# Performance work log

Hardware: AMD Instinct MI355X
Metric: run time of the kernel (lower is better)

Reference implementation:

```python
import jax, jax.numpy as jnp
import numpy as np

D = 1024      # n_embd
NH = 16       # attention heads
E = 8         # n_experts
K = 2         # k_best
FF = 4 * D    # expert MLP hidden
EPS = 1e-6    # rms_norm_epsilon
TEMP = 1.0    # target_temperature


def setup_inputs() -> dict:
    key = jax.random.key(0)
    ks = jax.random.split(key, 12)
    B, S = 2, 1024
    s = 0.02
    return {
        "x": jax.random.normal(ks[0], (B, S, D), jnp.float32),
        "attn_norm_w": jnp.ones((D,), jnp.float32),
        "wq": jax.random.normal(ks[1], (D, D), jnp.float32) * s,
        "wk": jax.random.normal(ks[2], (D, D), jnp.float32) * s,
        "wv": jax.random.normal(ks[3], (D, D), jnp.float32) * s,
        "wo": jax.random.normal(ks[4], (D, D), jnp.float32) * s,
        "mlp_norm_w": jnp.ones((D,), jnp.float32),
        "router_w": jax.random.normal(ks[5], (D, E), jnp.float32) * s,
        "w1": jax.random.normal(ks[6], (E, D, FF), jnp.float32) * s,
        "b1": jnp.zeros((E, FF), jnp.float32),
        "w2": jax.random.normal(ks[7], (E, FF, D), jnp.float32) * s,
        "b2": jnp.zeros((E, D), jnp.float32),
    }


def _rmsnorm(x, w):
    var = jnp.mean(jnp.square(x), axis=-1, keepdims=True)
    return x * jax.lax.rsqrt(var + EPS) * w


def _attention(x, wq, wk, wv, wo):
    B, S, _ = x.shape
    dh = D // NH
    q = (x @ wq).reshape(B, S, NH, dh)
    k = (x @ wk).reshape(B, S, NH, dh)
    v = (x @ wv).reshape(B, S, NH, dh)
    scores = jnp.einsum("bqhd,bkhd->bhqk", q, k) / jnp.sqrt(jnp.float32(dh))
    causal = jnp.tril(jnp.ones((S, S), bool))  # [S,S]
    scores = jnp.where(causal[None, None], scores, jnp.finfo(scores.dtype).min)
    attn = jax.nn.softmax(scores, axis=-1)
    out = jnp.einsum("bhqk,bkhd->bqhd", attn, v).reshape(B, S, D)
    return out @ wo


def reference(x, attn_norm_w, wq, wk, wv, wo, mlp_norm_w, router_w, w1, b1, w2, b2):
    B, S, _ = x.shape
    # attention sub-block
    x = x + _attention(_rmsnorm(x, attn_norm_w), wq, wk, wv, wo)
    residual = x
    h = _rmsnorm(x, mlp_norm_w)  # [B,S,D]

    # router: temperature softmax + top-k
    logits = h @ router_w / TEMP                      # [B,S,E]
    probs = jax.nn.softmax(logits, axis=-1)
    top_k_scores, top_k_indices = jax.lax.top_k(probs, K)  # [B,S,K]
    onehot = jax.nn.one_hot(top_k_indices, E, dtype=h.dtype)  # [B,S,K,E]
    gates = jnp.einsum("bsk,bske->bse", top_k_scores, onehot)  # [B,S,E]

    # load-balancing loss (Switch-style) + expert counts
    counts = jnp.sum(onehot, axis=(0, 1, 2))          # [E]
    frac = counts / (B * S * K)
    mean_prob = jnp.mean(probs, axis=(0, 1))          # [E]
    balancing_loss = E * jnp.sum(frac * mean_prob)

    # experts: dense dispatch; tokens with zero gate contribute nothing,
    # so this matches the sort/gather/scatter top-k combine exactly.
    pre = jnp.einsum("bsd,edf->ebsf", h, w1) + b1[:, None, None]  # [E,B,S,FF]
    act = jax.nn.gelu(pre)
    y = jnp.einsum("ebsf,efd->ebsd", act, w2) + b2[:, None, None]  # [E,B,S,D]
    moe = jnp.einsum("ebsd,bse->bsd", y, gates)

    out = residual + moe
    return out, balancing_loss, counts
```

## Files before the change

### kernel.cpp

```cpp
#include <hip/hip_runtime.h>

typedef __bf16 bf16;
typedef __bf16 bf16x4 __attribute__((ext_vector_type(4)));
typedef __bf16 bf16x8 __attribute__((ext_vector_type(8)));
typedef float f32x4 __attribute__((ext_vector_type(4)));

#define D_   1024
#define S_   1024
#define B_   2
#define NTOK 2048
#define FF_  4096
#define NE   8
#define CAP  5120
#define OUTN 2097152

__device__ __forceinline__ float gelu_f(float x) {
    float u = 0.7978845608028654f * (x + 0.044715f * x * x * x);
    float a = fabsf(u);
    float e = __expf(-2.0f * a);
    float t = (1.0f - e) / (1.0f + e);
    t = copysignf(t, u);
    return 0.5f * x * (1.0f + t);
}

__device__ __forceinline__ void gload16(const void* g, void* l) {
    __builtin_amdgcn_global_load_lds((const __attribute__((address_space(1))) unsigned int*)g,
                                     (__attribute__((address_space(3))) unsigned int*)l,
                                     16, 0, 0);
}

#define VMCNT(n) asm volatile("s_waitcnt vmcnt(" n ")" ::: "memory")
#define BARRIER() do { asm volatile("" ::: "memory"); \
                       __builtin_amdgcn_s_barrier();  \
                       asm volatile("" ::: "memory"); } while (0)

__global__ __launch_bounds__(256) void rmsnorm_k(const float* __restrict__ x,
                                                 const float* __restrict__ w,
                                                 float* __restrict__ yf,
                                                 bf16* __restrict__ yhi,
                                                 bf16* __restrict__ ylo) {
    int row = blockIdx.x;
    int t = threadIdx.x;
    const float* xr = x + (size_t)row * D_;
    float4 v = *(const float4*)(xr + t * 4);
    float ss = v.x * v.x + v.y * v.y + v.z * v.z + v.w * v.w;
    for (int off = 32; off; off >>= 1) ss += __shfl_down(ss, off);
    __shared__ float wsum[4];
    if ((t & 63) == 0) wsum[t >> 6] = ss;
    __syncthreads();
    float tot = wsum[0] + wsum[1] + wsum[2] + wsum[3];
    float rr = rsqrtf(tot * (1.0f / D_) + 1e-6f);
    float4 wv = *(const float4*)(w + t * 4);
    float y[4];
    y[0] = v.x * rr * wv.x; y[1] = v.y * rr * wv.y;
    y[2] = v.z * rr * wv.z; y[3] = v.w * rr * wv.w;
    if (yf) *(float4*)(yf + (size_t)row * D_ + t * 4) = *(float4*)y;
    if (yhi) {
#pragma unroll
        for (int i = 0; i < 4; i++) {
            bf16 hi = (bf16)y[i];
            yhi[(size_t)row * D_ + t * 4 + i] = hi;
            if (ylo) ylo[(size_t)row * D_ + t * 4 + i] = (bf16)(y[i] - (float)hi);
        }
    }
}

__global__ __launch_bounds__(256) void trans_split_k(
    const float* __restrict__ w0, const float* __restrict__ w1p,
    const float* __restrict__ w2p, const float* __restrict__ w3,
    bf16* o0h, bf16* o0l, bf16* o1h, bf16* o1l,
    bf16* o2h, bf16* o2l, bf16* o3h, bf16* o3l) {
    int z = blockIdx.z;
    const float* src = (z == 0) ? w0 : (z == 1) ? w1p : (z == 2) ? w2p : w3;
    bf16* dh = (z == 0) ? o0h : (z == 1) ? o1h : (z == 2) ? o2h : o3h;
    bf16* dl = (z == 0) ? o0l : (z == 1) ? o1l : (z == 2) ? o2l : o3l;
    __shared__ float tl[32][33];
    int c0 = blockIdx.x * 32, r0 = blockIdx.y * 32;
    int tx = threadIdx.x & 31, ty = threadIdx.x >> 5;
#pragma unroll
    for (int i = 0; i < 4; i++) {
        int r = ty + i * 8;
        tl[r][tx] = src[(size_t)(r0 + r) * 1024 + c0 + tx];
    }
    __syncthreads();
#pragma unroll
    for (int i = 0; i < 4; i++) {
        int c = ty + i * 8;
        float v = tl[tx][c];
        bf16 hi = (bf16)v;
        dh[(size_t)(c0 + c) * 1024 + r0 + tx] = hi;
        dl[(size_t)(c0 + c) * 1024 + r0 + tx] = (bf16)(v - (float)hi);
    }
}

__global__ __launch_bounds__(256) void transpose_cast4_k(const float* __restrict__ in,
                                                         bf16* __restrict__ out,
                                                         int R, int C) {
    __shared__ float tl[64][65];
    size_t base = (size_t)blockIdx.z * R * C;
    const float* src = in + base;
    bf16* dst = out + base;
    int c0 = blockIdx.x * 64, r0 = blockIdx.y * 64;
    int t = threadIdx.x;
    int lr = t >> 4;
    int lc = (t & 15) * 4;
#pragma unroll
    for (int i = 0; i < 4; i++) {
        int r = lr + i * 16;
        float4 v = *(const float4*)(src + (size_t)(r0 + r) * C + c0 + lc);
        tl[r][lc] = v.x; tl[r][lc + 1] = v.y; tl[r][lc + 2] = v.z; tl[r][lc + 3] = v.w;
    }
    __syncthreads();
    int wc = t >> 4;
    int wr = (t & 15) * 4;
#pragma unroll
    for (int i = 0; i < 4; i++) {
        int c = wc + i * 16;
        bf16x4 o;
        o[0] = (bf16)tl[wr][c];     o[1] = (bf16)tl[wr + 1][c];
        o[2] = (bf16)tl[wr + 2][c]; o[3] = (bf16)tl[wr + 3][c];
        *(bf16x4*)(dst + (size_t)(c0 + c) * R + r0 + wr) = o;
    }
}

#define SPLIT_STAGE(bi, k0)                             \
    gload16(gah0 + (k0), Lah[bi] + wv * 512);           \
    gload16(gah1 + (k0), Lah[bi] + 2048 + wv * 512);    \
    gload16(gal0 + (k0), Lal[bi] + wv * 512);           \
    gload16(gal1 + (k0), Lal[bi] + 2048 + wv * 512);    \
    gload16(gbh0 + (k0), Lbh[bi] + wv * 512);           \
    gload16(gbh1 + (k0), Lbh[bi] + 2048 + wv * 512);    \
    gload16(gbl0 + (k0), Lbl[bi] + wv * 512);           \
    gload16(gbl1 + (k0), Lbl[bi] + 2048 + wv * 512);

#define SPLIT_COMPUTE(bi) {                                                            \
    bf16x8 fah[4], fal[4], fbh[4], fbl[4];                                             \
    _Pragma("unroll") for (int i = 0; i < 4; i++) {                                    \
        fah[i] = *(const bf16x8*)(Lah[bi] + ra_off[i]);                                \
        fal[i] = *(const bf16x8*)(Lal[bi] + ra_off[i]);                                \
        fbh[i] = *(const bf16x8*)(Lbh[bi] + rb_off[i]);                                \
        fbl[i] = *(const bf16x8*)(Lbl[bi] + rb_off[i]);                                \
    }                                                                                  \
    _Pragma("unroll") for (int mt = 0; mt < 4; mt++)                                   \
    _Pragma("unroll") for (int nt = 0; nt < 4; nt++) {                                 \
        acc[mt][nt] = __builtin_amdgcn_mfma_f32_16x16x32_bf16(fah[mt], fbh[nt], acc[mt][nt], 0, 0, 0); \
        acc[mt][nt] = __builtin_amdgcn_mfma_f32_16x16x32_bf16(fah[mt], fbl[nt], acc[mt][nt], 0, 0, 0); \
        acc[mt][nt] = __builtin_amdgcn_mfma_f32_16x16x32_bf16(fal[mt], fbh[nt], acc[mt][nt], 0, 0, 0); \
    } }

#define SPLIT_STEP(bi, VM)          \
    VMCNT(VM);                      \
    BARRIER();                      \
    SPLIT_COMPUTE(bi);              \
    BARRIER();

#define SPLIT_DECLS(KOFF)                                                              \
    __shared__ __align__(16) bf16 Lah[2][4096];                                        \
    __shared__ __align__(16) bf16 Lal[2][4096];                                        \
    __shared__ __align__(16) bf16 Lbh[2][4096];                                        \
    __shared__ __align__(16) bf16 Lbl[2][4096];                                        \
    int t = threadIdx.x;                                                               \
    int wv = t >> 6, ln = t & 63;                                                      \
    int wm = wv >> 1, wn = wv & 1, l15 = ln & 15, qd = ln >> 4;                        \
    int sr0 = t >> 2, sr1 = 64 + sr0, cl = t & 3;                                      \
    int cs0 = (cl ^ ((sr0 >> 1) & 3)) * 8;                                             \
    int cs1 = (cl ^ ((sr1 >> 1) & 3)) * 8;                                             \
    const bf16* gah0 = Ah + (size_t)(m0 + sr0) * 1024 + (KOFF) + cs0;                  \
    const bf16* gah1 = Ah + (size_t)(m0 + sr1) * 1024 + (KOFF) + cs1;                  \
    const bf16* gal0 = Al + (size_t)(m0 + sr0) * 1024 + (KOFF) + cs0;                  \
    const bf16* gal1 = Al + (size_t)(m0 + sr1) * 1024 + (KOFF) + cs1;                  \
    const bf16* gbh0 = Bh + (size_t)(n0 + sr0) * 1024 + (KOFF) + cs0;                  \
    const bf16* gbh1 = Bh + (size_t)(n0 + sr1) * 1024 + (KOFF) + cs1;                  \
    const bf16* gbl0 = Bl + (size_t)(n0 + sr0) * 1024 + (KOFF) + cs0;                  \
    const bf16* gbl1 = Bl + (size_t)(n0 + sr1) * 1024 + (KOFF) + cs1;                  \
    int ra_off[4], rb_off[4];                                                          \
    _Pragma("unroll") for (int i = 0; i < 4; i++) {                                    \
        int r1 = wm * 64 + i * 16 + l15;                                               \
        ra_off[i] = r1 * 32 + (qd ^ ((r1 >> 1) & 3)) * 8;                              \
        int r2 = wn * 64 + i * 16 + l15;                                               \
        rb_off[i] = r2 * 32 + (qd ^ ((r2 >> 1) & 3)) * 8;                              \
    }                                                                                  \
    f32x4 acc[4][4];                                                                   \
    _Pragma("unroll") for (int mt = 0; mt < 4; mt++)                                   \
    _Pragma("unroll") for (int nt = 0; nt < 4; nt++) acc[mt][nt] = (f32x4){0.f,0.f,0.f,0.f};

__global__ __launch_bounds__(256) void gemm_qkv_k(
    const bf16* __restrict__ Ah, const bf16* __restrict__ Al,
    const bf16* __restrict__ Bqh, const bf16* __restrict__ Bql,
    const bf16* __restrict__ Bkh, const bf16* __restrict__ Bkl,
    const bf16* __restrict__ Bvh, const bf16* __restrict__ Bvl,
    bf16* Cqh, bf16* Cql, bf16* Ckh, bf16* Ckl, bf16* Cvh, bf16* Cvl) {
    int gy = blockIdx.y, zw = gy >> 3;
    const bf16* Bh = (zw == 0) ? Bqh : (zw == 1) ? Bkh : Bvh;
    const bf16* Bl = (zw == 0) ? Bql : (zw == 1) ? Bkl : Bvl;
    bf16* Ch = (zw == 0) ? Cqh : (zw == 1) ? Ckh : Cvh;
    bf16* Cl = (zw == 0) ? Cql : (zw == 1) ? Ckl : Cvl;
    int m0 = blockIdx.x * 128, n0 = (gy & 7) * 128;
    SPLIT_DECLS(0)
    SPLIT_STAGE(0, 0);
    for (int k0 = 0; k0 < 960; k0 += 64) {
        SPLIT_STAGE(1, k0 + 32);
        SPLIT_STEP(0, "8");
        SPLIT_STAGE(0, k0 + 64);
        SPLIT_STEP(1, "8");
    }
    SPLIT_STAGE(1, 992);
    SPLIT_STEP(0, "8");
    SPLIT_STEP(1, "0");
#pragma unroll
    for (int mt = 0; mt < 4; mt++)
#pragma unroll
        for (int nt = 0; nt < 4; nt++)
#pragma unroll
            for (int r = 0; r < 4; r++) {
                int gm = m0 + wm * 64 + mt * 16 + qd * 4 + r;
                int gn = n0 + wn * 64 + nt * 16 + l15;
                float vv = acc[mt][nt][r];
                bf16 hi = (bf16)vv;
                Ch[(size_t)gm * D_ + gn] = hi;
                Cl[(size_t)gm * D_ + gn] = (bf16)(vv - (float)hi);
            }
}

__global__ __launch_bounds__(256) void gemm_wo_k(
    const bf16* __restrict__ Ah, const bf16* __restrict__ Al,
    const bf16* __restrict__ Bh, const bf16* __restrict__ Bl,
    float* __restrict__ C) {
    int m0 = blockIdx.x * 128, n0 = blockIdx.y * 128;
    int kb = blockIdx.z * 256;
    SPLIT_DECLS(kb)
    SPLIT_STAGE(0, 0);
    for (int k0 = 0; k0 < 192; k0 += 64) {
        SPLIT_STAGE(1, k0 + 32);
        SPLIT_STEP(0, "8");
        SPLIT_STAGE(0, k0 + 64);
        SPLIT_STEP(1, "8");
    }
    SPLIT_STAGE(1, 224);
    SPLIT_STEP(0, "8");
    SPLIT_STEP(1, "0");
#pragma unroll
    for (int mt = 0; mt < 4; mt++)
#pragma unroll
        for (int nt = 0; nt < 4; nt++)
#pragma unroll
            for (int r = 0; r < 4; r++) {
                int gm = m0 + wm * 64 + mt * 16 + qd * 4 + r;
                int gn = n0 + wn * 64 + nt * 16 + l15;
                atomicAdd(&C[(size_t)gm * D_ + gn], acc[mt][nt][r]);
            }
}

#define AP 72

__global__ __launch_bounds__(256) void attn_mfma_k(
    const bf16* __restrict__ qhp, const bf16* __restrict__ qlp,
    const bf16* __restrict__ khp, const bf16* __restrict__ klp,
    const bf16* __restrict__ vhp, const bf16* __restrict__ vlp,
    bf16* __restrict__ aoh, bf16* __restrict__ aol) {
    int qt = (int)gridDim.x - 1 - (int)blockIdx.x;
    int h = blockIdx.y, b = blockIdx.z;
    __shared__ bf16 Ksh[64 * AP], Ksl[64 * AP], VTh[64 * AP], VTl[64 * AP];
    __shared__ bf16 Ph[4][16 * AP], Pl[4][16 * AP];
    int t = threadIdx.x, wv = t >> 6, ln = t & 63, l15 = ln & 15, qd = ln >> 4;

    bf16x8 aqh[2], aql[2];
    {
        size_t qb = ((size_t)(b * S_ + qt * 64 + wv * 16 + l15)) * D_ + h * 64 + qd * 8;
        aqh[0] = *(const bf16x8*)(qhp + qb);
        aqh[1] = *(const bf16x8*)(qhp + qb + 32);
        aql[0] = *(const bf16x8*)(qlp + qb);
        aql[1] = *(const bf16x8*)(qlp + qb + 32);
    }
    f32x4 oacc[4];
    float mrow[4], lrow[4];
#pragma unroll
    for (int i = 0; i < 4; i++) {
        oacc[i] = (f32x4){0.f, 0.f, 0.f, 0.f};
        mrow[i] = -1e30f; lrow[i] = 0.0f;
    }

    for (int kt = 0; kt <= qt; kt++) {
        __syncthreads();
#pragma unroll
        for (int j = 0; j < 2; j++) {
            int idx = t + j * 256;
            int row = idx >> 3, ch = (idx & 7) * 8;
            size_t g = ((size_t)(b * S_ + kt * 64 + row)) * D_ + h * 64 + ch;
            *(bf16x8*)&Ksh[row * AP + ch] = *(const bf16x8*)(khp + g);
            *(bf16x8*)&Ksl[row * AP + ch] = *(const bf16x8*)(klp + g);
            bf16x8 vvh = *(const bf16x8*)(vhp + g);
            bf16x8 vvl = *(const bf16x8*)(vlp + g);
#pragma unroll
            for (int jj = 0; jj < 8; jj++) {
                VTh[(ch + jj) * AP + row] = vvh[jj];
                VTl[(ch + jj) * AP + row] = vvl[jj];
            }
        }
        __syncthreads();

        f32x4 sacc[4];
#pragma unroll
        for (int nt = 0; nt < 4; nt++) sacc[nt] = (f32x4){0.f, 0.f, 0.f, 0.f};
#pragma unroll
        for (int ks = 0; ks < 2; ks++) {
#pragma unroll
            for (int nt = 0; nt < 4; nt++) {
                bf16x8 bh = *(const bf16x8*)&Ksh[(nt * 16 + l15) * AP + ks * 32 + qd * 8];
                bf16x8 bl = *(const bf16x8*)&Ksl[(nt * 16 + l15) * AP + ks * 32 + qd * 8];
                sacc[nt] = __builtin_amdgcn_mfma_f32_16x16x32_bf16(aqh[ks], bh, sacc[nt], 0, 0, 0);
                sacc[nt] = __builtin_amdgcn_mfma_f32_16x16x32_bf16(aqh[ks], bl, sacc[nt], 0, 0, 0);
                sacc[nt] = __builtin_amdgcn_mfma_f32_16x16x32_bf16(aql[ks], bh, sacc[nt], 0, 0, 0);
            }
        }
        bool diag = (kt == qt);
#pragma unroll
        for (int r = 0; r < 4; r++) {
            float s0[4];
#pragma unroll
            for (int nt = 0; nt < 4; nt++) {
                s0[nt] = sacc[nt][r] * 0.125f;
                if (diag && (nt * 16 + l15) > (wv * 16 + qd * 4 + r)) s0[nt] = -1e30f;
            }
            float vmax = fmaxf(fmaxf(s0[0], s0[1]), fmaxf(s0[2], s0[3]));
            for (int off = 1; off < 16; off <<= 1) vmax = fmaxf(vmax, __shfl_xor(vmax, off));
            float mnew = fmaxf(mrow[r], vmax);
            float alpha = __expf(mrow[r] - mnew);
            float p[4], rs = 0.0f;
#pragma unroll
            for (int nt = 0; nt < 4; nt++) { p[nt] = __expf(s0[nt] - mnew); rs += p[nt]; }
            for (int off = 1; off < 16; off <<= 1) rs += __shfl_xor(rs, off);
            lrow[r] = lrow[r] * alpha + rs;
            mrow[r] = mnew;
#pragma unroll
            for (int nt = 0; nt < 4; nt++) oacc[nt][r] *= alpha;
            int prow = qd * 4 + r;
#pragma unroll
            for (int nt = 0; nt < 4; nt++) {
                bf16 hi = (bf16)p[nt];
                Ph[wv][prow * AP + nt * 16 + l15] = hi;
                Pl[wv][prow * AP + nt * 16 + l15] = (bf16)(p[nt] - (float)hi);
            }
        }
#pragma unroll
        for (int ks2 = 0; ks2 < 2; ks2++) {
            bf16x8 aph = *(const bf16x8*)&Ph[wv][l15 * AP + ks2 * 32 + qd * 8];
            bf16x8 apl = *(const bf16x8*)&Pl[wv][l15 * AP + ks2 * 32 + qd * 8];
#pragma unroll
            for (int nt = 0; nt < 4; nt++) {
                bf16x8 bvh = *(const bf16x8*)&VTh[(nt * 16 + l15) * AP + ks2 * 32 + qd * 8];
                bf16x8 bvl = *(const bf16x8*)&VTl[(nt * 16 + l15) * AP + ks2 * 32 + qd * 8];
                oacc[nt] = __builtin_amdgcn_mfma_f32_16x16x32_bf16(aph, bvh, oacc[nt], 0, 0, 0);
                oacc[nt] = __builtin_amdgcn_mfma_f32_16x16x32_bf16(aph, bvl, oacc[nt], 0, 0, 0);
                oacc[nt] = __builtin_amdgcn_mfma_f32_16x16x32_bf16(apl, bvh, oacc[nt], 0, 0, 0);
            }
        }
    }

#pragma unroll
    for (int r = 0; r < 4; r++) {
        float inv = 1.0f / lrow[r];
        size_t rowa = ((size_t)(b * S_ + qt * 64 + wv * 16 + qd * 4 + r)) * D_ + h * 64;
#pragma unroll
        for (int nt = 0; nt < 4; nt++) {
            float o = oacc[nt][r] * inv;
            bf16 hi = (bf16)o;
            aoh[rowa + nt * 16 + l15] = hi;
            aol[rowa + nt * 16 + l15] = (bf16)(o - (float)hi);
        }
    }
}

__global__ __launch_bounds__(256) void router_k(const float* __restrict__ h,
                                                const float* __restrict__ rw,
                                                int* __restrict__ tidx,
                                                float* __restrict__ tgate,
                                                int* __restrict__ ecnt,
                                                float* __restrict__ psum) {
    int wv = threadIdx.x >> 6, ln = threadIdx.x & 63;
    int tok = blockIdx.x * 4 + wv;
    const float* hr = h + (size_t)tok * D_;
    float acc[NE];
#pragma unroll
    for (int e = 0; e < NE; e++) acc[e] = 0.0f;
    int base = ln * 16;
#pragma unroll
    for (int c = 0; c < 4; c++) {
        float4 hv = *(const float4*)(hr + base + c * 4);
        const float* rp = rw + (size_t)(base + c * 4) * NE;
        float hx[4] = {hv.x, hv.y, hv.z, hv.w};
#pragma unroll
        for (int jj = 0; jj < 4; jj++)
#pragma unroll
            for (int e = 0; e < NE; e++)
                acc[e] = fmaf(hx[jj], rp[jj * NE + e], acc[e]);
    }
#pragma unroll
    for (int e = 0; e < NE; e++)
        for (int off = 32; off; off >>= 1) acc[e] += __shfl_down(acc[e], off);

    __shared__ float pb[4][NE];
    if (ln == 0) {
        float mx = acc[0];
#pragma unroll
        for (int e = 1; e < NE; e++) mx = fmaxf(mx, acc[e]);
        float p[NE], ssum = 0.0f;
#pragma unroll
        for (int e = 0; e < NE; e++) { p[e] = expf(acc[e] - mx); ssum += p[e]; }
        float inv = 1.0f / ssum;
#pragma unroll
        for (int e = 0; e < NE; e++) p[e] *= inv;
        int i0 = 0; float b0 = p[0];
#pragma unroll
        for (int e = 1; e < NE; e++) if (p[e] > b0) { b0 = p[e]; i0 = e; }
        int i1 = -1; float b1v = -1.0f;
#pragma unroll
        for (int e = 0; e < NE; e++) if (e != i0 && p[e] > b1v) { b1v = p[e]; i1 = e; }
        tidx[tok * 2] = i0; tidx[tok * 2 + 1] = i1;
        tgate[tok * 2] = b0; tgate[tok * 2 + 1] = b1v;
        atomicAdd(&ecnt[i0], 1);
        atomicAdd(&ecnt[i1], 1);
#pragma unroll
        for (int e = 0; e < NE; e++) pb[wv][e] = p[e];
    }
    __syncthreads();
    if (threadIdx.x < NE) {
        float s2 = pb[0][threadIdx.x] + pb[1][threadIdx.x] + pb[2][threadIdx.x] + pb[3][threadIdx.x];
        atomicAdd(&psum[threadIdx.x], s2);
    }
}

__global__ void passb_k(const int* __restrict__ ecnt, const float* __restrict__ psum,
                        int* __restrict__ eoffp, int* __restrict__ ecnt2,
                        float* __restrict__ out_tail) {
    if (threadIdx.x == 0) {
        int off = 0; float loss = 0.0f;
        for (int e = 0; e < NE; e++) {
            eoffp[e] = off;
            int c = ecnt[e];
            off += (c + 127) & ~127;
            loss += (c * (1.0f / 4096.0f)) * (psum[e] * (1.0f / 2048.0f));
            out_tail[1 + e] = (float)c;
            ecnt2[e] = 0;
        }
        eoffp[NE] = off;
        out_tail[0] = 8.0f * loss;
    }
}

__global__ __launch_bounds__(256) void scatter_k(const int* __restrict__ tidx,
                                                 const int* __restrict__ eoffp,
                                                 int* __restrict__ ecnt2,
                                                 int* __restrict__ stok,
                                                 int* __restrict__ sidx) {
    int tok = blockIdx.x * 256 + threadIdx.x;
    for (int k = 0; k < 2; k++) {
        int e = tidx[tok * 2 + k];
        int pos = eoffp[e] + atomicAdd(&ecnt2[e], 1);
        stok[pos] = tok;
        sidx[tok * 2 + k] = pos;
    }
}

#define MOE_STAGE(bufA, bufB, k0)                       \
    gload16(ga0 + (k0), (bufA) + wv * 512);             \
    gload16(ga1 + (k0), (bufA) + 2048 + wv * 512);      \
    gload16(gb0 + (k0), (bufB) + wv * 512);             \
    gload16(gb1 + (k0), (bufB) + 2048 + wv * 512);

#define MOE_TILE(bufA, bufB) {                                                         \
    bf16x8 af[4], bfr[4];                                                              \
    _Pragma("unroll") for (int i = 0; i < 4; i++) {                                    \
        af[i]  = *(const bf16x8*)((bufA) + ra_off[i]);                                 \
        bfr[i] = *(const bf16x8*)((bufB) + rb_off[i]);                                 \
    }                                                                                  \
    _Pragma("unroll") for (int mt = 0; mt < 4; mt++)                                   \
    _Pragma("unroll") for (int nt = 0; nt < 4; nt++)                                   \
        acc[mt][nt] = __builtin_amdgcn_mfma_f32_16x16x32_bf16(af[mt], bfr[nt], acc[mt][nt], 0, 0, 0); }

#define MOE_STEP(rdA, rdB, VM)      \
    VMCNT(VM);                      \
    BARRIER();                      \
    MOE_TILE(rdA, rdB);             \
    BARRIER();

__global__ __launch_bounds__(256) void moe_gemm1_k(const bf16* __restrict__ hB,
                                                   const bf16* __restrict__ w1t,
                                                   const float* __restrict__ b1,
                                                   const int* __restrict__ eoffp,
                                                   const int* __restrict__ stok,
                                                   bf16* __restrict__ act) {
    int m0 = blockIdx.x * 128, n0 = blockIdx.y * 128;
    if (m0 >= eoffp[NE]) return;
    int e = 0;
#pragma unroll
    for (int i = 1; i < NE; i++) if (m0 >= eoffp[i]) e = i;

    __shared__ __align__(16) bf16 As[2][4096];
    __shared__ __align__(16) bf16 Bs[2][4096];
    int t = threadIdx.x;
    int wv = t >> 6, ln = t & 63;
    int wm = wv >> 1, wn = wv & 1, l15 = ln & 15, qd = ln >> 4;

    int sr0 = t >> 2, sr1 = 64 + sr0, cl = t & 3;
    int cs0 = (cl ^ ((sr0 >> 1) & 3)) * 8;
    int cs1 = (cl ^ ((sr1 >> 1) & 3)) * 8;
    const bf16* ga0 = hB + (size_t)stok[m0 + sr0] * D_ + cs0;
    const bf16* ga1 = hB + (size_t)stok[m0 + sr1] * D_ + cs1;
    const bf16* Bb = w1t + ((size_t)e * FF_ + n0) * D_;
    const bf16* gb0 = Bb + (size_t)sr0 * D_ + cs0;
    const bf16* gb1 = Bb + (size_t)sr1 * D_ + cs1;

    int ra_off[4], rb_off[4];
#pragma unroll
    for (int i = 0; i < 4; i++) {
        int r1 = wm * 64 + i * 16 + l15;
        ra_off[i] = r1 * 32 + (qd ^ ((r1 >> 1) & 3)) * 8;
        int r2 = wn * 64 + i * 16 + l15;
        rb_off[i] = r2 * 32 + (qd ^ ((r2 >> 1) & 3)) * 8;
    }

    f32x4 acc[4][4];
#pragma unroll
    for (int mt = 0; mt < 4; mt++)
#pragma unroll
        for (int nt = 0; nt < 4; nt++) acc[mt][nt] = (f32x4){0.f, 0.f, 0.f, 0.f};

    MOE_STAGE(As[0], Bs[0], 0);
    for (int k0 = 0; k0 < 960; k0 += 64) {
        MOE_STAGE(As[1], Bs[1], k0 + 32);
        MOE_STEP(As[0], Bs[0], "4");
        MOE_STAGE(As[0], Bs[0], k0 + 64);
        MOE_STEP(As[1], Bs[1], "4");
    }
    MOE_STAGE(As[1], Bs[1], 992);
    MOE_STEP(As[0], Bs[0], "4");
    MOE_STEP(As[1], Bs[1], "0");

    const float* b1e = b1 + (size_t)e * FF_;
#pragma unroll
    for (int mt = 0; mt < 4; mt++)
#pragma unroll
        for (int nt = 0; nt < 4; nt++) {
            int gn = n0 + wn * 64 + nt * 16 + l15;
            float bias = b1e[gn];
#pragma unroll
            for (int r = 0; r < 4; r++) {
                int gm = m0 + wm * 64 + mt * 16 + qd * 4 + r;
                act[(size_t)gm * FF_ + gn] = (bf16)gelu_f(acc[mt][nt][r] + bias);
            }
        }
}

__global__ __launch_bounds__(256) void moe_gemm2_k(const bf16* __restrict__ act,
                                                   const bf16* __restrict__ w2t,
                                                   const float* __restrict__ b2,
                                                   const int* __restrict__ eoffp,
                                                   float* __restrict__ y) {
    int m0 = blockIdx.x * 128, n0 = blockIdx.y * 128;
    if (m0 >= eoffp[NE]) return;
    int e = 0;
#pragma unroll
    for (int i = 1; i < NE; i++) if (m0 >= eoffp[i]) e = i;

    __shared__ __align__(16) bf16 As[4][4096];
    __shared__ __align__(16) bf16 Bs[4][4096];
    int t = threadIdx.x;
    int wv = t >> 6, ln = t & 63;
    int wm = wv >> 1, wn = wv & 1, l15 = ln & 15, qd = ln >> 4;

    int sr0 = t >> 2, sr1 = 64 + sr0, cl = t & 3;
    int cs0 = (cl ^ ((sr0 >> 1) & 3)) * 8;
    int cs1 = (cl ^ ((sr1 >> 1) & 3)) * 8;
    const bf16* ga0 = act + (size_t)(m0 + sr0) * FF_ + cs0;
    const bf16* ga1 = act + (size_t)(m0 + sr1) * FF_ + cs1;
    const bf16* Bb = w2t + ((size_t)e * D_ + n0) * FF_;
    const bf16* gb0 = Bb + (size_t)sr0 * FF_ + cs0;
    const bf16* gb1 = Bb + (size_t)sr1 * FF_ + cs1;

    int ra_off[4], rb_off[4];
#pragma unroll
    for (int i = 0; i < 4; i++) {
        int r1 = wm * 64 + i * 16 + l15;
        ra_off[i] = r1 * 32 + (qd ^ ((r1 >> 1) & 3)) * 8;
        int r2 = wn * 64 + i * 16 + l15;
        rb_off[i] = r2 * 32 + (qd ^ ((r2 >> 1) & 3)) * 8;
    }

    f32x4 acc[4][4];
#pragma unroll
    for (int mt = 0; mt < 4; mt++)
#pragma unroll
        for (int nt = 0; nt < 4; nt++) acc[mt][nt] = (f32x4){0.f, 0.f, 0.f, 0.f};

    MOE_STAGE(As[0], Bs[0], 0);
    MOE_STAGE(As[1], Bs[1], 32);
    for (int k0 = 0; k0 < 3968; k0 += 128) {
        MOE_STAGE(As[2], Bs[2], k0 + 64);  MOE_STEP(As[0], Bs[0], "8");
        MOE_STAGE(As[3], Bs[3], k0 + 96);  MOE_STEP(As[1], Bs[1], "8");
        MOE_STAGE(As[0], Bs[0], k0 + 128); MOE_STEP(As[2], Bs[2], "8");
        MOE_STAGE(As[1], Bs[1], k0 + 160); MOE_STEP(As[3], Bs[3], "8");
    }
    MOE_STAGE(As[2], Bs[2], 4032); MOE_STEP(As[0], Bs[0], "8");
    MOE_STAGE(As[3], Bs[3], 4064); MOE_STEP(As[1], Bs[1], "8");
    MOE_STEP(As[2], Bs[2], "4");
    MOE_STEP(As[3], Bs[3], "0");

    const float* b2e = b2 + (size_t)e * D_;
#pragma unroll
    for (int mt = 0; mt < 4; mt++)
#pragma unroll
        for (int nt = 0; nt < 4; nt++) {
            int gn = n0 + wn * 64 + nt * 16 + l15;
            float bias = b2e[gn];
#pragma unroll
            for (int r = 0; r < 4; r++) {
                int gm = m0 + wm * 64 + mt * 16 + qd * 4 + r;
                y[(size_t)gm * D_ + gn] = acc[mt][nt][r] + bias;
            }
        }
}

__global__ __launch_bounds__(256) void combine_k(const float* __restrict__ y,
                                                 const int* __restrict__ sidx,
                                                 const float* __restrict__ tgate,
                                                 float* __restrict__ out) {
    int tok = blockIdx.x;
    int d = threadIdx.x * 4;
    int s0 = sidx[tok * 2], s1 = sidx[tok * 2 + 1];
    float g0 = tgate[tok * 2], g1 = tgate[tok * 2 + 1];
    float4 a = *(const float4*)(y + (size_t)s0 * D_ + d);
    float4 b = *(const float4*)(y + (size_t)s1 * D_ + d);
    float4 o = *(const float4*)(out + (size_t)tok * D_ + d);
    o.x += g0 * a.x + g1 * b.x;
    o.y += g0 * a.y + g1 * b.y;
    o.z += g0 * a.z + g1 * b.z;
    o.w += g0 * a.w + g1 * b.w;
    *(float4*)(out + (size_t)tok * D_ + d) = o;
}

extern "C" void kernel_launch(void* const* d_in, const int* in_sizes, int n_in,
                              void* d_out, int out_size, void* d_ws, size_t ws_size,
                              hipStream_t stream) {
    const float* x   = (const float*)d_in[0];
    const float* anw = (const float*)d_in[1];
    const float* wq  = (const float*)d_in[2];
    const float* wk  = (const float*)d_in[3];
    const float* wv  = (const float*)d_in[4];
    const float* wo  = (const float*)d_in[5];
    const float* mnw = (const float*)d_in[6];
    const float* rw  = (const float*)d_in[7];
    const float* w1  = (const float*)d_in[8];
    const float* b1  = (const float*)d_in[9];
    const float* w2  = (const float*)d_in[10];
    const float* b2  = (const float*)d_in[11];
    float* out = (float*)d_out;

    char* p = (char*)d_ws;
    auto take = [&](size_t n) { char* r = p; p += (n + 255) & ~(size_t)255; return r; };
    bf16* h1h = (bf16*)take((size_t)OUTN * 2);
    bf16* h1l = (bf16*)take((size_t)OUTN * 2);
    bf16* qh  = (bf16*)take((size_t)OUTN * 2);
    bf16* ql  = (bf16*)take((size_t)OUTN * 2);
    bf16* kh  = (bf16*)take((size_t)OUTN * 2);
    bf16* kl  = (bf16*)take((size_t)OUTN * 2);
    bf16* vh  = (bf16*)take((size_t)OUTN * 2);
    bf16* vl  = (bf16*)take((size_t)OUTN * 2);
    bf16* wqth = (bf16*)take((size_t)D_ * D_ * 2);
    bf16* wqtl = (bf16*)take((size_t)D_ * D_ * 2);
    bf16* wkth = (bf16*)take((size_t)D_ * D_ * 2);
    bf16* wktl = (bf16*)take((size_t)D_ * D_ * 2);
    bf16* wvth = (bf16*)take((size_t)D_ * D_ * 2);
    bf16* wvtl = (bf16*)take((size_t)D_ * D_ * 2);
    bf16* woth = (bf16*)take((size_t)D_ * D_ * 2);
    bf16* wotl = (bf16*)take((size_t)D_ * D_ * 2);
    bf16* w1t = (bf16*)take((size_t)NE * FF_ * D_ * 2);
    bf16* w2t = (bf16*)take((size_t)NE * FF_ * D_ * 2);
    bf16* act = (bf16*)take((size_t)CAP * FF_ * 2);
    int*   tidx  = (int*)take(NTOK * 2 * 4);
    float* tgate = (float*)take(NTOK * 2 * 4);
    int*   sidx  = (int*)take(NTOK * 2 * 4);
    int*   ecnt  = (int*)take(64);
    int*   ecnt2 = (int*)take(64);
    float* psum  = (float*)take(64);
    int*   eoffp = (int*)take(64);
    int*   stok  = (int*)take(CAP * 4);

    bf16*  aoh = h1h;
    bf16*  aol = h1l;
    float* h_f = (float*)qh;
    bf16*  h_b = kh;
    float* y   = (float*)vh;

    hipMemsetAsync(ecnt, 0, NE * 4, stream);
    hipMemsetAsync(psum, 0, NE * 4, stream);
    hipMemsetAsync(stok, 0, CAP * 4, stream);
    hipMemcpyAsync(out, x, (size_t)OUTN * 4, hipMemcpyDeviceToDevice, stream);

    trans_split_k<<<dim3(32, 32, 4), 256, 0, stream>>>(wq, wk, wv, wo,
        wqth, wqtl, wkth, wktl, wvth, wvtl, woth, wotl);
    transpose_cast4_k<<<dim3(FF_ / 64, D_ / 64, NE), 256, 0, stream>>>(w1, w1t, D_, FF_);
    transpose_cast4_k<<<dim3(D_ / 64, FF_ / 64, NE), 256, 0, stream>>>(w2, w2t, FF_, D_);

    rmsnorm_k<<<NTOK, 256, 0, stream>>>(x, anw, nullptr, h1h, h1l);
    gemm_qkv_k<<<dim3(16, 24), 256, 0, stream>>>(h1h, h1l,
        wqth, wqtl, wkth, wktl, wvth, wvtl, qh, ql, kh, kl, vh, vl);
    attn_mfma_k<<<dim3(16, 16, 2), 256, 0, stream>>>(qh, ql, kh, kl, vh, vl, aoh, aol);
    gemm_wo_k<<<dim3(16, 8, 4), 256, 0, stream>>>(aoh, aol, woth, wotl, out);

    rmsnorm_k<<<NTOK, 256, 0, stream>>>(out, mnw, h_f, h_b, nullptr);
    router_k<<<NTOK / 4, 256, 0, stream>>>(h_f, rw, tidx, tgate, ecnt, psum);
    passb_k<<<1, 64, 0, stream>>>(ecnt, psum, eoffp, ecnt2, out + OUTN);
    scatter_k<<<NTOK / 256, 256, 0, stream>>>(tidx, eoffp, ecnt2, stok, sidx);
    moe_gemm1_k<<<dim3(CAP / 128, FF_ / 128), 256, 0, stream>>>(h_b, w1t, b1, eoffp, stok, act);
    moe_gemm2_k<<<dim3(CAP / 128, D_ / 128), 256, 0, stream>>>(act, w2t, b2, eoffp, y);
    combine_k<<<NTOK, 256, 0, stream>>>(y, sidx, tgate, out);
}
```

Measured before the change: 776.1 us.

## Pre-transpose V and use direct global-to-LDS swizzled loads in attention

Adds a separate kernel that writes V hi/lo in a transposed [b,h,d,s] layout. The attention kernel then loads K and transposed V tiles straight into LDS with gload16 and an XOR-swizzled layout, replacing the register-staged scalar transpose stores and the padded layout. This removes per-element LDS scatter writes and bank conflicts in the inner loop, at the cost of an extra kernel launch and about 8 MB of extra global traffic for the transposed V buffers.

```diff
diff --git a/kernel.cpp b/kernel.cpp
--- a/kernel.cpp
+++ b/kernel.cpp
@@ -120,6 +120,36 @@
         o[0] = (bf16)tl[wr][c];     o[1] = (bf16)tl[wr + 1][c];
         o[2] = (bf16)tl[wr + 2][c]; o[3] = (bf16)tl[wr + 3][c];
         *(bf16x4*)(dst + (size_t)(c0 + c) * R + r0 + wr) = o;
+    }
+}
+
+__global__ __launch_bounds__(256) void vtrans_k(const bf16* __restrict__ vh,
+                                                const bf16* __restrict__ vl,
+                                                bf16* __restrict__ vth,
+                                                bf16* __restrict__ vtl) {
+    int s0 = blockIdx.x * 64;
+    int bh = blockIdx.y;
+    int b = bh >> 4, h = bh & 15;
+    const bf16* src = blockIdx.z ? vl : vh;
+    bf16* dst = blockIdx.z ? vtl : vth;
+    __shared__ bf16 tl[64][65];
+    int t = threadIdx.x;
+    int lr = t >> 4, lc = (t & 15) * 4;
+#pragma unroll
+    for (int i = 0; i < 4; i++) {
+        int r = lr + i * 16;
+        bf16x4 v = *(const bf16x4*)(src + (size_t)(b * S_ + s0 + r) * D_ + h * 64 + lc);
+        tl[r][lc] = v[0]; tl[r][lc + 1] = v[1]; tl[r][lc + 2] = v[2]; tl[r][lc + 3] = v[3];
+    }
+    __syncthreads();
+    int wc = t >> 4, wr = (t & 15) * 4;
+#pragma unroll
+    for (int i = 0; i < 4; i++) {
+        int c = wc + i * 16;
+        bf16x4 o;
+        o[0] = tl[wr][c];     o[1] = tl[wr + 1][c];
+        o[2] = tl[wr + 2][c]; o[3] = tl[wr + 3][c];
+        *(bf16x4*)(dst + (size_t)(bh * 64 + c) * S_ + s0 + wr) = o;
     }
 }
 
@@ -256,11 +286,11 @@
 __global__ __launch_bounds__(256) void attn_mfma_k(
     const bf16* __restrict__ qhp, const bf16* __restrict__ qlp,
     const bf16* __restrict__ khp, const bf16* __restrict__ klp,
-    const bf16* __restrict__ vhp, const bf16* __restrict__ vlp,
+    const bf16* __restrict__ vth, const bf16* __restrict__ vtl,
     bf16* __restrict__ aoh, bf16* __restrict__ aol) {
     int qt = (int)gridDim.x - 1 - (int)blockIdx.x;
     int h = blockIdx.y, b = blockIdx.z;
-    __shared__ bf16 Ksh[64 * AP], Ksl[64 * AP], VTh[64 * AP], VTl[64 * AP];
+    __shared__ __align__(16) bf16 Ksh[4096], Ksl[4096], VTh[4096], VTl[4096];
     __shared__ bf16 Ph[4][16 * AP], Pl[4][16 * AP];
     int t = threadIdx.x, wv = t >> 6, ln = t & 63, l15 = ln & 15, qd = ln >> 4;
 
@@ -272,6 +302,27 @@
         aql[0] = *(const bf16x8*)(qlp + qb);
         aql[1] = *(const bf16x8*)(qlp + qb + 32);
     }
+
+    int srow = t >> 3, scl = t & 7;
+    int gsc = (scl ^ (srow & 7)) * 8;
+    const bf16* kh0 = khp + (size_t)(b * S_ + srow) * D_ + h * 64 + gsc;
+    const bf16* kh1 = khp + (size_t)(b * S_ + srow + 32) * D_ + h * 64 + gsc;
+    const bf16* kl0 = klp + (size_t)(b * S_ + srow) * D_ + h * 64 + gsc;
+    const bf16* kl1 = klp + (size_t)(b * S_ + srow + 32) * D_ + h * 64 + gsc;
+    const bf16* vt0 = vth + (size_t)((b * 16 + h) * 64 + srow) * S_ + gsc;
+    const bf16* vt1 = vth + (size_t)((b * 16 + h) * 64 + srow + 32) * S_ + gsc;
+    const bf16* wl0 = vtl + (size_t)((b * 16 + h) * 64 + srow) * S_ + gsc;
+    const bf16* wl1 = vtl + (size_t)((b * 16 + h) * 64 + srow + 32) * S_ + gsc;
+
+    int soff[4][2];
+#pragma unroll
+    for (int nt = 0; nt < 4; nt++)
+#pragma unroll
+        for (int ks = 0; ks < 2; ks++) {
+            int r = nt * 16 + l15;
+            soff[nt][ks] = r * 64 + ((ks * 4 + qd) ^ (r & 7)) * 8;
+        }
+
     f32x4 oacc[4];
     float mrow[4], lrow[4];
 #pragma unroll
@@ -281,23 +332,15 @@
     }
 
     for (int kt = 0; kt <= qt; kt++) {
-        __syncthreads();
-#pragma unroll
-        for (int j = 0; j < 2; j++) {
-            int idx = t + j * 256;
-            int row = idx >> 3, ch = (idx & 7) * 8;
-            size_t g = ((size_t)(b * S_ + kt * 64 + row)) * D_ + h * 64 + ch;
-            *(bf16x8*)&Ksh[row * AP + ch] = *(const bf16x8*)(khp + g);
-            *(bf16x8*)&Ksl[row * AP + ch] = *(const bf16x8*)(klp + g);
-            bf16x8 vvh = *(const bf16x8*)(vhp + g);
-            bf16x8 vvl = *(const bf16x8*)(vlp + g);
-#pragma unroll
-            for (int jj = 0; jj < 8; jj++) {
-                VTh[(ch + jj) * AP + row] = vvh[jj];
-                VTl[(ch + jj) * AP + row] = vvl[jj];
-            }
-        }
-        __syncthreads();
+        BARRIER();
+        size_t ko = (size_t)kt * 64 * D_;
+        int vo = kt * 64;
+        gload16(kh0 + ko, Ksh + wv * 512); gload16(kh1 + ko, Ksh + 2048 + wv * 512);
+        gload16(kl0 + ko, Ksl + wv * 512); gload16(kl1 + ko, Ksl + 2048 + wv * 512);
+        gload16(vt0 + vo, VTh + wv * 512); gload16(vt1 + vo, VTh + 2048 + wv * 512);
+        gload16(wl0 + vo, VTl + wv * 512); gload16(wl1 + vo, VTl + 2048 + wv * 512);
+        VMCNT("0");
+        BARRIER();
 
         f32x4 sacc[4];
 #pragma unroll
@@ -306,8 +349,8 @@
         for (int ks = 0; ks < 2; ks++) {
 #pragma unroll
             for (int nt = 0; nt < 4; nt++) {
-                bf16x8 bh = *(const bf16x8*)&Ksh[(nt * 16 + l15) * AP + ks * 32 + qd * 8];
-                bf16x8 bl = *(const bf16x8*)&Ksl[(nt * 16 + l15) * AP + ks * 32 + qd * 8];
+                bf16x8 bh = *(const bf16x8*)&Ksh[soff[nt][ks]];
+                bf16x8 bl = *(const bf16x8*)&Ksl[soff[nt][ks]];
                 sacc[nt] = __builtin_amdgcn_mfma_f32_16x16x32_bf16(aqh[ks], bh, sacc[nt], 0, 0, 0);
                 sacc[nt] = __builtin_amdgcn_mfma_f32_16x16x32_bf16(aqh[ks], bl, sacc[nt], 0, 0, 0);
                 sacc[nt] = __builtin_amdgcn_mfma_f32_16x16x32_bf16(aql[ks], bh, sacc[nt], 0, 0, 0);
@@ -348,8 +391,8 @@
             bf16x8 apl = *(const bf16x8*)&Pl[wv][l15 * AP + ks2 * 32 + qd * 8];
 #pragma unroll
             for (int nt = 0; nt < 4; nt++) {
-                bf16x8 bvh = *(const bf16x8*)&VTh[(nt * 16 + l15) * AP + ks2 * 32 + qd * 8];
-                bf16x8 bvl = *(const bf16x8*)&VTl[(nt * 16 + l15) * AP + ks2 * 32 + qd * 8];
+                bf16x8 bvh = *(const bf16x8*)&VTh[soff[nt][ks2]];
+                bf16x8 bvl = *(const bf16x8*)&VTl[soff[nt][ks2]];
                 oacc[nt] = __builtin_amdgcn_mfma_f32_16x16x32_bf16(aph, bvh, oacc[nt], 0, 0, 0);
                 oacc[nt] = __builtin_amdgcn_mfma_f32_16x16x32_bf16(aph, bvl, oacc[nt], 0, 0, 0);
                 oacc[nt] = __builtin_amdgcn_mfma_f32_16x16x32_bf16(apl, bvh, oacc[nt], 0, 0, 0);
@@ -666,6 +709,8 @@
     bf16* kl  = (bf16*)take((size_t)OUTN * 2);
     bf16* vh  = (bf16*)take((size_t)OUTN * 2);
     bf16* vl  = (bf16*)take((size_t)OUTN * 2);
+    bf16* vth = (bf16*)take((size_t)OUTN * 2);
+    bf16* vtl = (bf16*)take((size_t)OUTN * 2);
     bf16* wqth = (bf16*)take((size_t)D_ * D_ * 2);
     bf16* wqtl = (bf16*)take((size_t)D_ * D_ * 2);
     bf16* wkth = (bf16*)take((size_t)D_ * D_ * 2);
@@ -705,7 +750,8 @@
     rmsnorm_k<<<NTOK, 256, 0, stream>>>(x, anw, nullptr, h1h, h1l);
     gemm_qkv_k<<<dim3(16, 24), 256, 0, stream>>>(h1h, h1l,
         wqth, wqtl, wkth, wktl, wvth, wvtl, qh, ql, kh, kl, vh, vl);
-    attn_mfma_k<<<dim3(16, 16, 2), 256, 0, stream>>>(qh, ql, kh, kl, vh, vl, aoh, aol);
+    vtrans_k<<<dim3(S_ / 64, 32, 2), 256, 0, stream>>>(vh, vl, vth, vtl);
+    attn_mfma_k<<<dim3(16, 16, 2), 256, 0, stream>>>(qh, ql, kh, kl, vth, vtl, aoh, aol);
     gemm_wo_k<<<dim3(16, 8, 4), 256, 0, stream>>>(aoh, aol, woth, wotl, out);
 
     rmsnorm_k<<<NTOK, 256, 0, stream>>>(out, mnw, h_f, h_b, nullptr);
```

New measurement: 742.3 us. 1.05x faster.
